# Kernel tuning notes

Measured on AMD Instinct MI355X. Metric: run time of the kernel, lower is better.

The kernel has to match this reference:

```python
import jax, jax.numpy as jnp
import numpy as np

B = 512          # batch
G = 16           # groups in conv_transpose
N_SUB = 8        # sub-images per sample (384 / (3*G))
CIN = 64         # A_in_channel (per-sample conv_transpose input channels)
S_SZ = 5         # ica_ssize = kernel = stride of conv_transpose


def _conv_w(k, shape):
    fan_in = shape[1] * shape[2] * shape[3]
    return jax.random.normal(k, shape, jnp.float32) / np.sqrt(fan_in).astype(np.float32)


def setup_inputs() -> dict:
    key = jax.random.key(0)
    ks = jax.random.split(key, 8)
    A = jax.random.normal(ks[0], (B, 512, 2, 2), jnp.float32)
    S = jax.random.normal(ks[1], (B, CIN, 3, S_SZ, S_SZ), jnp.float32)
    W1 = _conv_w(ks[2], (384, 384, 3, 3)); b1 = jnp.zeros((384,), jnp.float32)
    W2 = _conv_w(ks[3], (384, 384, 3, 3)); b2 = jnp.zeros((384,), jnp.float32)
    W3 = _conv_w(ks[4], (512, 384, 3, 3)); b3 = jnp.zeros((512,), jnp.float32)
    W4 = _conv_w(ks[5], (512, 512, 5, 5)); b4 = jnp.zeros((512,), jnp.float32)
    Wl = jax.random.normal(ks[6], (10, 512), jnp.float32) / np.sqrt(512).astype(np.float32)
    bl = jnp.zeros((10,), jnp.float32)
    return {"A": A, "S": S, "W1": W1, "b1": b1, "W2": W2, "b2": b2,
            "W3": W3, "b3": b3, "W4": W4, "b4": b4, "Wl": Wl, "bl": bl}


def _conv_relu(x, w, b, stride, pad):
    y = jax.lax.conv_general_dilated(
        x, w, window_strides=(stride, stride),
        padding=[(pad, pad), (pad, pad)],
        dimension_numbers=("NCHW", "OIHW", "NCHW"))
    return jax.nn.relu(y + b[None, :, None, None])


def reference(A, S, W1, b1, W2, b2, W3, b3, W4, b4, Wl, bl):
    # Per-sample grouped conv_transpose2d with stride == kernel size on a 2x2
    # input: output s x s blocks do not overlap, so it is a pure einsum.
    # A: (B, 512, 2, 2) -> (B, n_sub=8, groups=16, cpg=4, 2, 2)
    # S: (B, 64, 3, 5, 5) -> (B, groups=16, cpg=4, 3, 5, 5)
    cpg = CIN // G  # 4 in-channels per group
    A6 = A.reshape(B, N_SUB, G, cpg, 2, 2)
    S6 = S.reshape(B, G, cpg, 3, S_SZ, S_SZ)
    # out[b,n,g,o, h*s+p, w*s+q] = sum_c A[b,n,g,c,h,w] * S[b,g,c,o,p,q]
    x = jnp.einsum("bngchw,bgcopq->bngohpwq", A6, S6)
    x = x.reshape(B, N_SUB * G * 3, 2 * S_SZ, 2 * S_SZ)  # (B, 384, 10, 10)

    x = _conv_relu(x, W1, b1, stride=1, pad=1)   # (B, 384, 10, 10)
    x = _conv_relu(x, W2, b2, stride=2, pad=1)   # (B, 384, 5, 5)
    x = _conv_relu(x, W3, b3, stride=1, pad=1)   # (B, 512, 5, 5)
    x = _conv_relu(x, W4, b4, stride=1, pad=0)   # (B, 512, 1, 1)

    x = x.reshape(B, -1)                         # (B, 512)
    return x @ Wl.T + bl                         # (B, 10)
```

## Files before the change

### kernel.cpp

```cpp
#include <hip/hip_runtime.h>
#include <hip/hip_bf16.h>


typedef __attribute__((ext_vector_type(8))) short bf16x8;
typedef __attribute__((ext_vector_type(4))) float f32x4;

__device__ __forceinline__ short round_bf16(float v) {
    __hip_bfloat16 h = __float2bfloat16(v);
    return __builtin_bit_cast(short, h);
}

__device__ __forceinline__ int xcd_swizzle(int bid, int total) {
    int q = total >> 3, r = total & 7;
    int xcd = bid & 7, idx = bid >> 3;
    return (xcd < r ? xcd * (q + 1) : r * (q + 1) + (xcd - r) * q) + idx;
}

template<int HP, int C>
__global__ void zero_border(short* __restrict__ p, int Bc)
{
    constexpr int NB = 2 * HP + 2 * (HP - 2);
    constexpr int C8 = C / 8;
    int idx = blockIdx.x * blockDim.x + threadIdx.x;
    int total = Bc * NB * C8;
    if (idx >= total) return;
    int c8 = idx % C8;
    int t  = idx / C8;
    int pb = t % NB;
    int b  = t / NB;
    int r, c;
    if (pb < HP)          { r = 0;      c = pb; }
    else if (pb < 2 * HP) { r = HP - 1; c = pb - HP; }
    else { int s = pb - 2 * HP; r = 1 + (s >> 1); c = (s & 1) ? HP - 1 : 0; }
    size_t d = (((size_t)b * HP + r) * HP + c) * C + c8 * 8;
    *(bf16x8*)&p[d] = (bf16x8){0, 0, 0, 0, 0, 0, 0, 0};
}

__global__ void pack_w_frag_h(const float* __restrict__ W,
                              short* __restrict__ wh, int total)
{
    int idx = blockIdx.x * blockDim.x + threadIdx.x;
    if (idx >= total) return;
    int oc = idx / 3456, r = idx - oc * 3456;
    int t = r / 384, ic = r - t * 384;
    float v = W[((size_t)oc * 384 + ic) * 9 + t];
    int g16 = oc >> 4, l15 = oc & 15;
    int c = ic >> 5, kg = (ic >> 3) & 3, e = ic & 7;
    size_t d = (((size_t)g16 * 108 + (t * 12 + c)) * 64 + kg * 16 + l15) * 8 + e;
    wh[d] = round_bf16(v);
}

__global__ void pack_w4_frag_h(const float* __restrict__ W,
                               short* __restrict__ wh, int total)
{
    int idx = blockIdx.x * blockDim.x + threadIdx.x;
    if (idx >= total) return;
    int oc = idx / 12800, k = idx - oc * 12800;
    int g16 = oc >> 4, l15 = oc & 15;
    int s = k >> 5, kg = (k >> 3) & 3, e = k & 7;
    size_t d = (((size_t)g16 * 400 + s) * 64 + kg * 16 + l15) * 8 + e;
    wh[d] = round_bf16(W[idx]);
}

__global__ void __launch_bounds__(384)
einsum_pack3(const float* __restrict__ A, const float* __restrict__ S,
             short* __restrict__ oh)
{
    __shared__ float sS[4800];
    const int b  = blockIdx.x;
    const int ch = threadIdx.x;

    const float4* S4 = (const float4*)(S + (size_t)b * 4800);
    for (int i = threadIdx.x; i < 1200; i += 384)
        ((float4*)sS)[i] = S4[i];

    const int n = ch / 48, rr = ch - n * 48;
    const int g = rr / 3,  o = rr - g * 3;

    const float4* A4 = (const float4*)(A + (size_t)b * 2048) + (n * 64 + g * 4);
    float4 av0 = A4[0], av1 = A4[1], av2 = A4[2], av3 = A4[3];

    __syncthreads();

    const float* Sb = sS + g * 300 + o * 25;

    #pragma unroll
    for (int h = 0; h < 2; ++h) {
        #pragma unroll
        for (int w = 0; w < 2; ++w) {
            const float a0 = (h == 0 && w == 0) ? av0.x : (h == 0 && w == 1) ? av0.y
                           : (h == 1 && w == 0) ? av0.z : av0.w;
            const float a1 = (h == 0 && w == 0) ? av1.x : (h == 0 && w == 1) ? av1.y
                           : (h == 1 && w == 0) ? av1.z : av1.w;
            const float a2 = (h == 0 && w == 0) ? av2.x : (h == 0 && w == 1) ? av2.y
                           : (h == 1 && w == 0) ? av2.z : av2.w;
            const float a3 = (h == 0 && w == 0) ? av3.x : (h == 0 && w == 1) ? av3.y
                           : (h == 1 && w == 0) ? av3.z : av3.w;
            size_t dbase = ((size_t)(b * 12 + h * 5 + 1) * 12 + (w * 5 + 1)) * 384 + ch;
            #pragma unroll
            for (int pp = 0; pp < 5; ++pp) {
                #pragma unroll
                for (int q = 0; q < 5; ++q) {
                    const int soff = pp * 5 + q;
                    float s = a0 * Sb[soff] + a1 * Sb[75 + soff]
                            + a2 * Sb[150 + soff] + a3 * Sb[225 + soff];
                    oh[dbase + (size_t)(pp * 12 + q) * 384] = round_bf16(s);
                }
            }
        }
    }
}

template<int OC_T, int HOUT, int HPIN, int HPOUT, int STRIDE, int MODE, int NT,
         int NSAMP, int DBUF>
__global__ void __launch_bounds__(256)
conv_mfma5(const short* __restrict__ in_h, const short* __restrict__ wph,
           const float* __restrict__ bias, short* __restrict__ out_h)
{
    constexpr int IC = 384;
    constexpr int NS = 108;
    constexpr int NF = NT / 32;
    constexpr int PIX = HOUT * HOUT;
    constexpr int M_BLK = NSAMP * PIX;
    constexpr int PROWS = NSAMP * HPIN * HPIN;
    constexpr int G = OC_T / NT;
    constexpr int NU = (PROWS * 2 + 255) / 256;
    constexpr int BUFSZ = PROWS * 40;
    __shared__ short s_a[(DBUF ? 2 : 1) * BUFSZ];

    const int swz = xcd_swizzle(blockIdx.x, gridDim.x);
    const int mt = swz / G;
    const int g  = swz % G;
    const int n0 = g * NT;
    const int bb0 = mt * NSAMP;

    const int tid = threadIdx.x;
    const int lane = tid & 63;
    const int wid  = tid >> 6;
    const int wm = (wid & 1) * 64;
    const int wn = (wid >> 1) * (NT / 2);
    const int l15 = lane & 15, kg = lane >> 4;

    size_t usrc[NU]; int udst[NU]; bool uval[NU];
    #pragma unroll
    for (int j = 0; j < NU; ++j) {
        int u = tid + j * 256;
        int row = u >> 1, hf = u & 1;
        uval[j] = row < PROWS;
        int rc = uval[j] ? row : 0;
        int sN = rc / (HPIN * HPIN), rr = rc % (HPIN * HPIN);
        usrc[j] = ((size_t)(bb0 + sN) * (HPIN * HPIN) + rr) * IC + hf * 16;
        udst[j] = rc * 40 + hf * 16;
    }

    int prow[4];
    #pragma unroll
    for (int mf = 0; mf < 4; ++mf) {
        int p = wm + mf * 16 + l15;
        int pc = p < M_BLK ? p : M_BLK - 1;
        int sN = pc / PIX, pr = pc % PIX;
        int py = pr / HOUT, px = pr - py * HOUT;
        prow[mf] = sN * (HPIN * HPIN) + py * STRIDE * HPIN + px * STRIDE;
    }

    const short* wb = wph + (size_t)((n0 + wn) >> 4) * (NS * 512) + lane * 8;

    f32x4 acc[4][NF];
    #pragma unroll
    for (int i = 0; i < 4; ++i)
        #pragma unroll
        for (int j = 0; j < NF; ++j)
            acc[i][j] = (f32x4){0.f, 0.f, 0.f, 0.f};

    bf16x8 sreg[NU][2];
    auto loadG = [&](int c) {
        #pragma unroll
        for (int j = 0; j < NU; ++j) if (uval[j]) {
            const short* src = in_h + usrc[j] + c * 32;
            sreg[j][0] = *(const bf16x8*)src;
            sreg[j][1] = *(const bf16x8*)(src + 8);
        }
    };
    auto writeL = [&](int off) {
        #pragma unroll
        for (int j = 0; j < NU; ++j) if (uval[j]) {
            *(bf16x8*)&s_a[off + udst[j]]     = sreg[j][0];
            *(bf16x8*)&s_a[off + udst[j] + 8] = sreg[j][1];
        }
    };
    auto compute = [&](int c, int off) {
        bf16x8 bcur[NF], bnxt[NF];
        #pragma unroll
        for (int nf = 0; nf < NF; ++nf)
            bcur[nf] = *(const bf16x8*)(wb + (size_t)nf * (NS * 512) + (size_t)c * 512);
        #pragma unroll
        for (int t = 0; t < 9; ++t) {
            if (t < 8) {
                #pragma unroll
                for (int nf = 0; nf < NF; ++nf)
                    bnxt[nf] = *(const bf16x8*)(wb + (size_t)nf * (NS * 512)
                                                + (size_t)((t + 1) * 12 + c) * 512);
            }
            const int troff = (t / 3) * HPIN + (t % 3);
            bf16x8 af[4];
            #pragma unroll
            for (int mf = 0; mf < 4; ++mf)
                af[mf] = *(const bf16x8*)&s_a[off + (prow[mf] + troff) * 40 + kg * 8];
            __builtin_amdgcn_s_setprio(1);
            #pragma unroll
            for (int nf = 0; nf < NF; ++nf)
                #pragma unroll
                for (int mf = 0; mf < 4; ++mf)
                    acc[mf][nf] = __builtin_amdgcn_mfma_f32_16x16x32_bf16(
                        af[mf], bcur[nf], acc[mf][nf], 0, 0, 0);
            __builtin_amdgcn_s_setprio(0);
            #pragma unroll
            for (int nf = 0; nf < NF; ++nf) bcur[nf] = bnxt[nf];
        }
    };

    if (DBUF) {
        loadG(0); writeL(0);
        __syncthreads();
        int buf = 0;
        for (int c = 0; c < 12; ++c) {
            if (c + 1 < 12) loadG(c + 1);
            compute(c, buf * BUFSZ);
            if (c + 1 < 12) writeL((buf ^ 1) * BUFSZ);
            __syncthreads();
            buf ^= 1;
        }
    } else {
        loadG(0);
        for (int c = 0; c < 12; ++c) {
            if (c) __syncthreads();
            writeL(0);
            __syncthreads();
            if (c + 1 < 12) loadG(c + 1);
            compute(c, 0);
        }
    }

    #pragma unroll
    for (int nf = 0; nf < NF; ++nf) {
        const int oc = n0 + wn + nf * 16 + l15;
        const float bv = bias[oc];
        #pragma unroll
        for (int mf = 0; mf < 4; ++mf) {
            #pragma unroll
            for (int j = 0; j < 4; ++j) {
                int p_out = wm + mf * 16 + kg * 4 + j;
                if (p_out < M_BLK) {
                    float v = acc[mf][nf][j] + bv;
                    v = v > 0.f ? v : 0.f;
                    int b2 = bb0 + p_out / PIX;
                    int pr2 = p_out % PIX;
                    if (MODE == 0) {
                        int y2 = pr2 / HOUT, x2 = pr2 - y2 * HOUT;
                        size_t d = ((size_t)(b2 * HPOUT + y2 + 1) * HPOUT + (x2 + 1)) * OC_T + oc;
                        out_h[d] = round_bf16(v);
                    } else {
                        out_h[((size_t)b2 * OC_T + oc) * PIX + pr2] = round_bf16(v);
                    }
                }
            }
        }
    }
}

template<int KS>
__global__ void __launch_bounds__(256)
gemm4_mfma3(const short* __restrict__ Ah, const short* __restrict__ wph,
            float* __restrict__ Cpart, int M)
{
    constexpr int NS4 = 400;
    constexpr int NSTEP = NS4 / KS;
    __shared__ short s_a[2][128 * 40];
    const int tid = threadIdx.x;
    const int nM = (M + 127) / 128;
    const int ks = blockIdx.x / (nM * 4);
    const int rb = blockIdx.x % (nM * 4);
    const int M0 = (rb / 4) * 128;
    const int n0 = (rb % 4) * 128;

    const int lane = tid & 63;
    const int wid  = tid >> 6;
    const int wm = (wid & 1) * 64;
    const int wn = (wid >> 1) * 64;
    const int l15 = lane & 15, kg = lane >> 4;

    const int arow = tid >> 1, ahf = tid & 1;
    int P = M0 + arow; if (P >= M) P = M - 1;
    const short* abase = Ah + (size_t)P * 12800 + ahf * 16;
    const int adst = arow * 40 + ahf * 16;

    const short* wbh = wph + (size_t)((n0 + wn) >> 4) * (NS4 * 512) + lane * 8;

    f32x4 acc[4][4];
    #pragma unroll
    for (int i = 0; i < 4; ++i)
        #pragma unroll
        for (int j = 0; j < 4; ++j)
            acc[i][j] = (f32x4){0.f, 0.f, 0.f, 0.f};

    auto stageA = [&](int j, int buf) {
        const short* src = abase + (size_t)(ks * NSTEP + j) * 32;
        *(bf16x8*)&s_a[buf][adst]     = *(const bf16x8*)src;
        *(bf16x8*)&s_a[buf][adst + 8] = *(const bf16x8*)(src + 8);
    };
    auto loadB = [&](int j, bf16x8 (&bh)[4]) {
        #pragma unroll
        for (int nf = 0; nf < 4; ++nf)
            bh[nf] = *(const bf16x8*)(wbh + (size_t)nf * (NS4 * 512)
                                      + (size_t)(ks * NSTEP + j) * 512);
    };
    auto compute = [&](const bf16x8 (&bh)[4], int buf) {
        bf16x8 af[4];
        #pragma unroll
        for (int mf = 0; mf < 4; ++mf)
            af[mf] = *(const bf16x8*)&s_a[buf][(wm + mf * 16 + l15) * 40 + kg * 8];
        __builtin_amdgcn_s_setprio(1);
        #pragma unroll
        for (int nf = 0; nf < 4; ++nf)
            #pragma unroll
            for (int mf = 0; mf < 4; ++mf)
                acc[mf][nf] = __builtin_amdgcn_mfma_f32_16x16x32_bf16(
                    af[mf], bh[nf], acc[mf][nf], 0, 0, 0);
        __builtin_amdgcn_s_setprio(0);
    };

    bf16x8 bhA[4], bhB[4];
    stageA(0, 0);
    loadB(0, bhA);
    __syncthreads();
    for (int jp = 0; jp < NSTEP; jp += 2) {
        stageA(jp + 1, 1);
        loadB(jp + 1, bhB);
        compute(bhA, 0);
        __syncthreads();
        if (jp + 2 < NSTEP) { stageA(jp + 2, 0); loadB(jp + 2, bhA); }
        compute(bhB, 1);
        __syncthreads();
    }

    float* cp = Cpart + (size_t)ks * M * 512;
    #pragma unroll
    for (int nf = 0; nf < 4; ++nf) {
        const int n = n0 + wn + nf * 16 + l15;
        #pragma unroll
        for (int mf = 0; mf < 4; ++mf) {
            #pragma unroll
            for (int j = 0; j < 4; ++j) {
                int m = M0 + wm + mf * 16 + kg * 4 + j;
                if (m < M) cp[(size_t)m * 512 + n] = acc[mf][nf][j];
            }
        }
    }
}

template<int KS>
__global__ void splitk_reduce_relu(const float* __restrict__ Cpart,
                                   const float* __restrict__ bias,
                                   float* __restrict__ out, int M, int N)
{
    int idx = blockIdx.x * blockDim.x + threadIdx.x;
    if (idx >= M * N) return;
    int oc = idx % N;
    float s = bias[oc];
    #pragma unroll
    for (int ks = 0; ks < KS; ++ks)
        s += Cpart[(size_t)ks * M * N + idx];
    out[idx] = s > 0.f ? s : 0.f;
}

__global__ void linear_naive(const float* __restrict__ x, const float* __restrict__ Wl,
                             const float* __restrict__ bl,
                             float* __restrict__ out, int total)
{
    int idx = blockIdx.x * blockDim.x + threadIdx.x;
    if (idx >= total) return;
    int b = idx / 10, j = idx - b * 10;
    const float* xb = x  + (size_t)b * 512;
    const float* wj = Wl + (size_t)j * 512;
    float s = bl[j];
    for (int k = 0; k < 512; ++k)
        s += xb[k] * wj[k];
    out[idx] = s;
}

extern "C" void kernel_launch(void* const* d_in, const int* in_sizes, int n_in,
                              void* d_out, int out_size, void* d_ws, size_t ws_size,
                              hipStream_t stream)
{
    const float* A  = (const float*)d_in[0];
    const float* S  = (const float*)d_in[1];
    const float* W1 = (const float*)d_in[2];
    const float* b1 = (const float*)d_in[3];
    const float* W2 = (const float*)d_in[4];
    const float* b2 = (const float*)d_in[5];
    const float* W3 = (const float*)d_in[6];
    const float* b3 = (const float*)d_in[7];
    const float* W4 = (const float*)d_in[8];
    const float* b4 = (const float*)d_in[9];
    const float* Wl = (const float*)d_in[10];
    const float* bl = (const float*)d_in[11];
    float* outp = (float*)d_out;
    char* base = (char*)d_ws;

    const int Btot = 512;
    constexpr int KS = 25;

    const size_t W12N = (size_t)384 * 3456;
    const size_t W3N  = (size_t)512 * 3456;
    const size_t W4N  = (size_t)512 * 12800;
    size_t off = 0;
    short* w1h = (short*)(base + off); off += W12N * 2;
    short* w2h = (short*)(base + off); off += W12N * 2;
    short* w3h = (short*)(base + off); off += W3N * 2;
    short* w4h = (short*)(base + off); off += W4N * 2;
    const size_t wreg = off;

    const size_t PS = 337664;
    int Bc = 512;
    while (Bc > 8 && wreg + (size_t)Bc * PS > ws_size) Bc >>= 1;

    pack_w_frag_h<<<(int)((W12N + 255) / 256), 256, 0, stream>>>(W1, w1h, (int)W12N);
    pack_w_frag_h<<<(int)((W12N + 255) / 256), 256, 0, stream>>>(W2, w2h, (int)W12N);
    pack_w_frag_h<<<(int)((W3N  + 255) / 256), 256, 0, stream>>>(W3, w3h, (int)W3N);
    pack_w4_frag_h<<<(int)((W4N + 255) / 256), 256, 0, stream>>>(W4, w4h, (int)W4N);

    size_t o2 = wreg;
    short* x0h = (short*)(base + o2); o2 += (size_t)Bc * 110592;
    short* x1h = (short*)(base + o2); o2 += (size_t)Bc * 110592;
    short* x2h = (short*)(base + o2); o2 += (size_t)Bc * 37632;
    short* x3h = (short*)(base + o2); o2 += (size_t)Bc * 25600;
    float* cp  = (float*)(base + o2); o2 += (size_t)Bc * (KS * 512 * 4);
    float* x4  = (float*)(base + o2);

    {
        int t0 = Bc * 44 * 48;
        zero_border<12, 384><<<(t0 + 255) / 256, 256, 0, stream>>>(x0h, Bc);
        zero_border<12, 384><<<(t0 + 255) / 256, 256, 0, stream>>>(x1h, Bc);
        int t2 = Bc * 24 * 48;
        zero_border<7, 384><<<(t2 + 255) / 256, 256, 0, stream>>>(x2h, Bc);
    }

    for (int b0 = 0; b0 < Btot; b0 += Bc) {
        einsum_pack3<<<dim3(Bc), 384, 0, stream>>>(
            A + (size_t)b0 * 2048, S + (size_t)b0 * 4800, x0h);

        conv_mfma5<384, 10, 12, 12, 1, 0, 128, 1, 1>
            <<<dim3(Bc * 3), 256, 0, stream>>>(x0h, w1h, b1, x1h);

        conv_mfma5<384, 5, 12, 7, 2, 0, 64, 4, 0>
            <<<dim3((Bc / 4) * 6), 256, 0, stream>>>(x1h, w2h, b2, x2h);

        conv_mfma5<512, 5, 7, 1, 1, 1, 128, 4, 1>
            <<<dim3((Bc / 4) * 4), 256, 0, stream>>>(x2h, w3h, b3, x3h);

        int nM = (Bc + 127) / 128;
        gemm4_mfma3<KS><<<dim3(KS * nM * 4), 256, 0, stream>>>(
            x3h, w4h, cp, Bc);
        int tr = Bc * 512;
        splitk_reduce_relu<KS><<<(tr + 255) / 256, 256, 0, stream>>>(
            cp, b4, x4, Bc, 512);

        int t5 = Bc * 10;
        linear_naive<<<(t5 + 255) / 256, 256, 0, stream>>>(
            x4, Wl, bl, outp + (size_t)b0 * 10, t5);
    }
}
```

Measured before the change: 427.5 us.

## Vectorize weight packing, pipeline B-fragment loads across chunks, retile conv2

The weight packing kernels now have each thread build and store a full 8-element bf16 vector, replacing one scalar store per element. For W4 the source reads also become float4 loads. In the conv kernel, the first weight fragment of the next input-channel chunk is prefetched during the last tap of the current chunk, so the pipeline no longer stalls at chunk boundaries. Conv2 moves from an N tile of 64 to 96, using 4 blocks per batch group instead of 6. That trades fewer, larger blocks against more registers per thread and possibly lower occupancy.

```diff
diff --git a/kernel.cpp b/kernel.cpp
--- a/kernel.cpp
+++ b/kernel.cpp
@@ -36,30 +36,42 @@
     *(bf16x8*)&p[d] = (bf16x8){0, 0, 0, 0, 0, 0, 0, 0};
 }
 
-__global__ void pack_w_frag_h(const float* __restrict__ W,
-                              short* __restrict__ wh, int total)
+__global__ void pack_w_frag_h8(const float* __restrict__ W,
+                               short* __restrict__ wh, int total8)
 {
     int idx = blockIdx.x * blockDim.x + threadIdx.x;
-    if (idx >= total) return;
-    int oc = idx / 3456, r = idx - oc * 3456;
-    int t = r / 384, ic = r - t * 384;
-    float v = W[((size_t)oc * 384 + ic) * 9 + t];
+    if (idx >= total8) return;
+    int oc = idx / 432, r = idx - oc * 432;
+    int t = r / 48, ic8 = r - t * 48;
+    int ic = ic8 * 8;
+    bf16x8 out;
+    #pragma unroll
+    for (int e = 0; e < 8; ++e)
+        out[e] = round_bf16(W[((size_t)oc * 384 + ic + e) * 9 + t]);
     int g16 = oc >> 4, l15 = oc & 15;
-    int c = ic >> 5, kg = (ic >> 3) & 3, e = ic & 7;
-    size_t d = (((size_t)g16 * 108 + (t * 12 + c)) * 64 + kg * 16 + l15) * 8 + e;
-    wh[d] = round_bf16(v);
-}
-
-__global__ void pack_w4_frag_h(const float* __restrict__ W,
-                               short* __restrict__ wh, int total)
+    int c = ic >> 5, kg = (ic >> 3) & 3;
+    size_t d = (((size_t)g16 * 108 + (t * 12 + c)) * 64 + kg * 16 + l15) * 8;
+    *(bf16x8*)&wh[d] = out;
+}
+
+__global__ void pack_w4_frag_h8(const float* __restrict__ W,
+                                short* __restrict__ wh, int total8)
 {
     int idx = blockIdx.x * blockDim.x + threadIdx.x;
-    if (idx >= total) return;
-    int oc = idx / 12800, k = idx - oc * 12800;
+    if (idx >= total8) return;
+    int oc = idx / 1600, k8 = idx - oc * 1600;
+    int k = k8 * 8;
+    const float4 f0 = *(const float4*)&W[(size_t)oc * 12800 + k];
+    const float4 f1 = *(const float4*)&W[(size_t)oc * 12800 + k + 4];
+    bf16x8 out;
+    out[0] = round_bf16(f0.x); out[1] = round_bf16(f0.y);
+    out[2] = round_bf16(f0.z); out[3] = round_bf16(f0.w);
+    out[4] = round_bf16(f1.x); out[5] = round_bf16(f1.y);
+    out[6] = round_bf16(f1.z); out[7] = round_bf16(f1.w);
     int g16 = oc >> 4, l15 = oc & 15;
-    int s = k >> 5, kg = (k >> 3) & 3, e = k & 7;
-    size_t d = (((size_t)g16 * 400 + s) * 64 + kg * 16 + l15) * 8 + e;
-    wh[d] = round_bf16(W[idx]);
+    int s = k >> 5, kg = (k >> 3) & 3;
+    size_t d = (((size_t)g16 * 400 + s) * 64 + kg * 16 + l15) * 8;
+    *(bf16x8*)&wh[d] = out;
 }
 
 __global__ void __launch_bounds__(384)
@@ -188,19 +200,17 @@
             *(bf16x8*)&s_a[off + udst[j] + 8] = sreg[j][1];
         }
     };
-    auto compute = [&](int c, int off) {
-        bf16x8 bcur[NF], bnxt[NF];
+    auto loadB = [&](int s, bf16x8 (&bh)[NF]) {
         #pragma unroll
         for (int nf = 0; nf < NF; ++nf)
-            bcur[nf] = *(const bf16x8*)(wb + (size_t)nf * (NS * 512) + (size_t)c * 512);
+            bh[nf] = *(const bf16x8*)(wb + (size_t)nf * (NS * 512) + (size_t)s * 512);
+    };
+    auto compute = [&](int c, int off, bf16x8 (&bcur)[NF]) {
+        bf16x8 bnxt[NF];
         #pragma unroll
         for (int t = 0; t < 9; ++t) {
-            if (t < 8) {
-                #pragma unroll
-                for (int nf = 0; nf < NF; ++nf)
-                    bnxt[nf] = *(const bf16x8*)(wb + (size_t)nf * (NS * 512)
-                                                + (size_t)((t + 1) * 12 + c) * 512);
-            }
+            const int sn = (t < 8) ? ((t + 1) * 12 + c) : (c < 11 ? (c + 1) : 0);
+            loadB(sn, bnxt);
             const int troff = (t / 3) * HPIN + (t % 3);
             bf16x8 af[4];
             #pragma unroll
@@ -219,13 +229,16 @@
         }
     };
 
+    bf16x8 bpipe[NF];
+    loadB(0, bpipe);
+
     if (DBUF) {
         loadG(0); writeL(0);
         __syncthreads();
         int buf = 0;
         for (int c = 0; c < 12; ++c) {
             if (c + 1 < 12) loadG(c + 1);
-            compute(c, buf * BUFSZ);
+            compute(c, buf * BUFSZ, bpipe);
             if (c + 1 < 12) writeL((buf ^ 1) * BUFSZ);
             __syncthreads();
             buf ^= 1;
@@ -237,7 +250,7 @@
             writeL(0);
             __syncthreads();
             if (c + 1 < 12) loadG(c + 1);
-            compute(c, 0);
+            compute(c, 0, bpipe);
         }
     }
 
@@ -424,10 +437,10 @@
     int Bc = 512;
     while (Bc > 8 && wreg + (size_t)Bc * PS > ws_size) Bc >>= 1;
 
-    pack_w_frag_h<<<(int)((W12N + 255) / 256), 256, 0, stream>>>(W1, w1h, (int)W12N);
-    pack_w_frag_h<<<(int)((W12N + 255) / 256), 256, 0, stream>>>(W2, w2h, (int)W12N);
-    pack_w_frag_h<<<(int)((W3N  + 255) / 256), 256, 0, stream>>>(W3, w3h, (int)W3N);
-    pack_w4_frag_h<<<(int)((W4N + 255) / 256), 256, 0, stream>>>(W4, w4h, (int)W4N);
+    pack_w_frag_h8<<<(int)((W12N / 8 + 255) / 256), 256, 0, stream>>>(W1, w1h, (int)(W12N / 8));
+    pack_w_frag_h8<<<(int)((W12N / 8 + 255) / 256), 256, 0, stream>>>(W2, w2h, (int)(W12N / 8));
+    pack_w_frag_h8<<<(int)((W3N  / 8 + 255) / 256), 256, 0, stream>>>(W3, w3h, (int)(W3N / 8));
+    pack_w4_frag_h8<<<(int)((W4N / 8 + 255) / 256), 256, 0, stream>>>(W4, w4h, (int)(W4N / 8));
 
     size_t o2 = wreg;
     short* x0h = (short*)(base + o2); o2 += (size_t)Bc * 110592;
@@ -452,8 +465,8 @@
         conv_mfma5<384, 10, 12, 12, 1, 0, 128, 1, 1>
             <<<dim3(Bc * 3), 256, 0, stream>>>(x0h, w1h, b1, x1h);
 
-        conv_mfma5<384, 5, 12, 7, 2, 0, 64, 4, 0>
-            <<<dim3((Bc / 4) * 6), 256, 0, stream>>>(x1h, w2h, b2, x2h);
+        conv_mfma5<384, 5, 12, 7, 2, 0, 96, 4, 0>
+            <<<dim3((Bc / 4) * 4), 256, 0, stream>>>(x1h, w2h, b2, x2h);
 
         conv_mfma5<512, 5, 7, 1, 1, 1, 128, 4, 1>
             <<<dim3((Bc / 4) * 4), 256, 0, stream>>>(x2h, w3h, b3, x3h);
```

Result: faster. 406.3 us (-5.0%).
